# Kernel tuning notes

Hardware: AMD Instinct MI355X
Metric: run time of the kernel (lower is better)

## Reference

```python
import jax, jax.numpy as jnp
import numpy as np
from jax import lax

L_TAU = 0.8
NUM_TIME = 20
B, H, W = 128, 64, 64
FLAT = 6 * 27 * 27  # 4374 features after conv(k=10)->55x55 and maxpool2 -> 27x27

def setup_inputs() -> dict:
    key = jax.random.key(0)
    k1, k2, k3, k4, k5, k6 = jax.random.split(key, 6)
    x = jax.random.uniform(k1, (B, H * W, NUM_TIME), dtype=jnp.float32)
    y = jax.random.randint(k2, (B,), 0, 2, dtype=jnp.int64)
    Wc = jax.random.normal(k3, (6, 1, 10, 10), dtype=jnp.float32) * 0.1  # OIHW
    bc = jnp.zeros((6,), dtype=jnp.float32)
    W2 = jax.random.normal(k4, (FLAT, 2), dtype=jnp.float32) * (1.0 / np.sqrt(FLAT))
    b2 = jnp.zeros((2,), dtype=jnp.float32)
    return {"x": x, "y": y, "Wc": Wc, "bc": bc, "W2": W2, "b2": b2}

def _maxpool2(a):
    return lax.reduce_window(a, -jnp.inf, lax.max,
                             (1, 1, 2, 2), (1, 1, 2, 2), 'VALID')

def _snu_forward(x, Wc, bc, W2, b2):
    xt = jnp.transpose(x, (2, 0, 1)).reshape(NUM_TIME, B, 1, H, W)  # [T,B,1,64,64]
    s1 = jnp.zeros((B, 6, 55, 55), jnp.float32); y1 = jnp.zeros_like(s1)
    s2 = jnp.zeros((B, 2), jnp.float32);        y2 = jnp.zeros_like(s2)

    def step(carry, x_t):
        s1, y1, s2, y2 = carry
        c = lax.conv_general_dilated(x_t, Wc, (1, 1), 'VALID',
                                     dimension_numbers=('NCHW', 'OIHW', 'NCHW'))
        # SNU state: s = relu(conv(x) + l_tau * s * (1 - y)); emission: y = sigmoid(s + b)
        s1 = jax.nn.relu(c + L_TAU * s1 * (1.0 - y1))
        y1 = jax.nn.sigmoid(s1 + bc[None, :, None, None])
        h = _maxpool2(y1).reshape(B, FLAT)           # [B, 4374]
        s2 = jax.nn.relu(h @ W2 + L_TAU * s2 * (1.0 - y2))
        y2 = jax.nn.sigmoid(s2 + b2)
        return (s1, y1, s2, y2), y2

    _, outs = lax.scan(step, (s1, y1, s2, y2), xt)   # [T, B, 2]
    out_rec = jnp.concatenate([jnp.zeros((1, B, 2), jnp.float32), outs], axis=0)
    out_rec = jnp.transpose(out_rec, (1, 0, 2))      # [B, T+1, 2]
    m = jnp.sum(out_rec, axis=1) / 20.0
    return m, out_rec

def reference(x, y, Wc, bc, W2, b2):
    m, out_rec = _snu_forward(x, Wc, bc, W2, b2)
    logp = jax.nn.log_softmax(m, axis=1)
    loss = -jnp.mean(logp[jnp.arange(B), y])         # CrossEntropyLoss
    acc = jnp.mean((jnp.argmax(m, axis=1) == y).astype(jnp.float32))
    return (loss, m, out_rec, acc)
```

## Files before the change

kernel.cpp:

```cpp
#include <hip/hip_runtime.h>
#include <hip/hip_bf16.h>
#include <math.h>

#define L_TAU_C 0.8f

__device__ __forceinline__ float sigmoidf_(float x) {
    return 1.0f / (1.0f + __expf(-x));
}

__global__ __launch_bounds__(256) void k_transpose(const float* __restrict__ x,
                                                   float* __restrict__ xT) {
    int gp = blockIdx.x * 256 + threadIdx.x;
    int b = gp >> 12, p = gp & 4095;
    const float4* src = reinterpret_cast<const float4*>(x + (size_t)gp * 20);
    float v[20];
#pragma unroll
    for (int k = 0; k < 5; ++k) {
        float4 q = src[k];
        v[4 * k + 0] = q.x; v[4 * k + 1] = q.y; v[4 * k + 2] = q.z; v[4 * k + 3] = q.w;
    }
    float* dst = xT + (size_t)b * 20 * 4096 + p;
#pragma unroll
    for (int t = 0; t < 20; ++t) dst[(size_t)t * 4096] = v[t];
}

__global__ __launch_bounds__(256) void k_conv_snu(
    const float* __restrict__ xT,
    const float* __restrict__ x,
    const float* __restrict__ Wc,
    const float* __restrict__ bc,
    const float* __restrict__ W2,
    float* __restrict__ part,
    int use_xT)
{
    __shared__ float xs[64 * 68];
    __shared__ float wsh[10 * 12];
    __shared__ float red[8];

    const int tid = threadIdx.x;
    const int bi = blockIdx.x;
    const int xcd = bi & 7, slot = bi >> 3;
    const int b = (slot / 6) * 8 + xcd;
    const int ch = slot % 6;

    if (tid < 100) wsh[(tid / 10) * 12 + (tid % 10)] = Wc[ch * 100 + tid];

    const bool active = tid < 243;
    const int r = tid / 9;
    const int cg = tid % 9;
    const int row0 = r * 2, col0 = cg * 6;

    float s1[2][6], y1[2][6];
#pragma unroll
    for (int i = 0; i < 2; ++i)
#pragma unroll
        for (int j = 0; j < 6; ++j) { s1[i][j] = 0.f; y1[i][j] = 0.f; }

    const float bch = bc[ch];

    float w2r[3][2];
#pragma unroll
    for (int pj = 0; pj < 3; ++pj) { w2r[pj][0] = 0.f; w2r[pj][1] = 0.f; }
    if (active) {
        int f0 = ch * 729 + r * 27 + cg * 3;
#pragma unroll
        for (int pj = 0; pj < 3; ++pj) {
            w2r[pj][0] = W2[(size_t)(f0 + pj) * 2 + 0];
            w2r[pj][1] = W2[(size_t)(f0 + pj) * 2 + 1];
        }
    }

    for (int t = 0; t < 20; ++t) {
        __syncthreads();
        if (use_xT) {
            const float4* src = reinterpret_cast<const float4*>(
                xT + ((size_t)b * 20 + t) * 4096);
#pragma unroll
            for (int k = 0; k < 4; ++k) {
                float4 v = src[tid + k * 256];
                int p = (tid + k * 256) * 4;
                int row = p >> 6, col = p & 63;
                *reinterpret_cast<float4*>(&xs[row * 68 + col]) = v;
            }
        } else {
#pragma unroll
            for (int k = 0; k < 16; ++k) {
                int p = tid + k * 256;
                xs[(p >> 6) * 68 + (p & 63)] = x[((size_t)b * 4096 + p) * 20 + t];
            }
        }
        __syncthreads();

        float p0 = 0.f, p1 = 0.f;
        if (active) {
            float c0[6], c1[6];
#pragma unroll
            for (int j = 0; j < 6; ++j) { c0[j] = 0.f; c1[j] = 0.f; }
            float wprev[10];
#pragma unroll
            for (int xr = 0; xr < 11; ++xr) {
                float seg[15];
                const float* xrow = &xs[(row0 + xr) * 68 + col0];
#pragma unroll
                for (int j = 0; j < 15; ++j) seg[j] = xrow[j];
                float wcur[10];
                if (xr <= 9) {
#pragma unroll
                    for (int kc = 0; kc < 10; ++kc) wcur[kc] = wsh[xr * 12 + kc];
#pragma unroll
                    for (int kc = 0; kc < 10; ++kc)
#pragma unroll
                        for (int j = 0; j < 6; ++j) c0[j] += seg[j + kc] * wcur[kc];
                }
                if (xr >= 1) {
#pragma unroll
                    for (int kc = 0; kc < 10; ++kc)
#pragma unroll
                        for (int j = 0; j < 6; ++j) c1[j] += seg[j + kc] * wprev[kc];
                }
                if (xr <= 9) {
#pragma unroll
                    for (int kc = 0; kc < 10; ++kc) wprev[kc] = wcur[kc];
                }
            }
#pragma unroll
            for (int j = 0; j < 6; ++j) {
                float sa = fmaxf(c0[j] + L_TAU_C * s1[0][j] * (1.f - y1[0][j]), 0.f);
                float sb = fmaxf(c1[j] + L_TAU_C * s1[1][j] * (1.f - y1[1][j]), 0.f);
                s1[0][j] = sa; s1[1][j] = sb;
                y1[0][j] = sigmoidf_(sa + bch);
                y1[1][j] = sigmoidf_(sb + bch);
            }
#pragma unroll
            for (int pj = 0; pj < 3; ++pj) {
                float h = fmaxf(fmaxf(y1[0][2 * pj], y1[0][2 * pj + 1]),
                                fmaxf(y1[1][2 * pj], y1[1][2 * pj + 1]));
                p0 += h * w2r[pj][0];
                p1 += h * w2r[pj][1];
            }
        }
#pragma unroll
        for (int off = 32; off >= 1; off >>= 1) {
            p0 += __shfl_down(p0, off);
            p1 += __shfl_down(p1, off);
        }
        int wave = tid >> 6;
        if ((tid & 63) == 0) { red[wave * 2] = p0; red[wave * 2 + 1] = p1; }
        __syncthreads();
        if (tid == 0) {
            float q0 = red[0] + red[2] + red[4] + red[6];
            float q1 = red[1] + red[3] + red[5] + red[7];
            float* dst = part + ((size_t)t * 128 + b) * 12 + ch * 2;
            dst[0] = q0; dst[1] = q1;
        }
    }
}

__global__ __launch_bounds__(128) void k_final(const float* __restrict__ part,
                                               const void* __restrict__ yraw,
                                               const float* __restrict__ b2,
                                               float* __restrict__ out) {
    __shared__ float red[4];
    const int b = threadIdx.x;

    const int* yi = (const int*)yraw;
    bool i64 = true;
    for (int k = 0; k < 64; ++k) {
        if (yi[2 * k + 1] != 0) { i64 = false; break; }
    }
    int lbl = i64 ? (int)((const long long*)yraw)[b] : yi[b];

    float b20 = b2[0], b21 = b2[1];
    float s20 = 0.f, s21 = 0.f, y20 = 0.f, y21 = 0.f, m0 = 0.f, m1 = 0.f;
    float* orec = out + 257 + b * 42;
    orec[0] = 0.f; orec[1] = 0.f;
    for (int t = 0; t < 20; ++t) {
        const float4* pp = reinterpret_cast<const float4*>(part + ((size_t)t * 128 + b) * 12);
        float4 a = pp[0], c = pp[1], d = pp[2];
        float sum0 = a.x + a.z + c.x + c.z + d.x + d.z;
        float sum1 = a.y + a.w + c.y + c.w + d.y + d.w;
        s20 = fmaxf(sum0 + L_TAU_C * s20 * (1.f - y20), 0.f);
        s21 = fmaxf(sum1 + L_TAU_C * s21 * (1.f - y21), 0.f);
        y20 = sigmoidf_(s20 + b20);
        y21 = sigmoidf_(s21 + b21);
        orec[(t + 1) * 2 + 0] = y20;
        orec[(t + 1) * 2 + 1] = y21;
        m0 += y20; m1 += y21;
    }
    m0 *= 0.05f; m1 *= 0.05f;
    out[1 + b * 2 + 0] = m0;
    out[1 + b * 2 + 1] = m1;

    float mx = fmaxf(m0, m1);
    float lse = mx + logf(expf(m0 - mx) + expf(m1 - mx));
    float lossc = -(((lbl != 0) ? m1 : m0) - lse);
    int pred = (m1 > m0) ? 1 : 0;
    float accc = (pred == lbl) ? 1.f : 0.f;
#pragma unroll
    for (int off = 32; off >= 1; off >>= 1) {
        lossc += __shfl_down(lossc, off);
        accc += __shfl_down(accc, off);
    }
    if ((b & 63) == 0) { red[(b >> 6) * 2] = lossc; red[(b >> 6) * 2 + 1] = accc; }
    __syncthreads();
    if (b == 0) {
        out[0] = (red[0] + red[2]) * (1.f / 128.f);
        out[5633] = (red[1] + red[3]) * (1.f / 128.f);
    }
}

extern "C" void kernel_launch(void* const* d_in, const int* in_sizes, int n_in,
                              void* d_out, int out_size, void* d_ws, size_t ws_size,
                              hipStream_t stream) {
    const float* x  = (const float*)d_in[0];
    const void*  y  = d_in[1];
    const float* Wc = (const float*)d_in[2];
    const float* bc = (const float*)d_in[3];
    const float* W2 = (const float*)d_in[4];
    const float* b2 = (const float*)d_in[5];
    float* out = (float*)d_out;

    const size_t xT_floats = (size_t)128 * 20 * 4096;
    const size_t need = (xT_floats + 20 * 128 * 6 * 2) * 4;
    const int use_xT = (ws_size >= need) ? 1 : 0;

    float* xT = (float*)d_ws;
    float* part = use_xT ? ((float*)d_ws + xT_floats) : (float*)d_ws;

    if (use_xT) {
        k_transpose<<<2048, 256, 0, stream>>>(x, xT);
    }
    k_conv_snu<<<768, 256, 0, stream>>>(xT, x, Wc, bc, W2, part, use_xT);
    k_final<<<1, 128, 0, stream>>>(part, y, b2, out);
}
```

Before: 182.6 us.

## Store transposed input in fp16, widen conv tile to 8 columns with swizzled LDS

The transpose kernel now writes the time-major input copy as fp16, halving the workspace traffic, and the conv kernel converts it back to fp32 when loading shared memory. The conv tile per thread grows from 6 to 8 output columns, so a block runs 189 active threads out of 192 instead of 243 of 256. Shared memory drops its row padding in favour of an XOR swizzle with float4 reads, and the filter weights are read straight from global memory (likely scalar loads) instead of through LDS. Rounding the input to fp16 introduces precision error in the conv, and thread 188's last tile reads past the 64-column row, relying on the masked column being unused.

```diff
diff --git a/kernel.cpp b/kernel.cpp
--- a/kernel.cpp
+++ b/kernel.cpp
@@ -4,12 +4,14 @@
 
 #define L_TAU_C 0.8f
 
+typedef __attribute__((ext_vector_type(8))) _Float16 half8_t;
+
 __device__ __forceinline__ float sigmoidf_(float x) {
     return 1.0f / (1.0f + __expf(-x));
 }
 
-__global__ __launch_bounds__(256) void k_transpose(const float* __restrict__ x,
-                                                   float* __restrict__ xT) {
+__global__ __launch_bounds__(256) void k_transpose16(const float* __restrict__ x,
+                                                     _Float16* __restrict__ xT) {
     int gp = blockIdx.x * 256 + threadIdx.x;
     int b = gp >> 12, p = gp & 4095;
     const float4* src = reinterpret_cast<const float4*>(x + (size_t)gp * 20);
@@ -19,23 +21,23 @@
         float4 q = src[k];
         v[4 * k + 0] = q.x; v[4 * k + 1] = q.y; v[4 * k + 2] = q.z; v[4 * k + 3] = q.w;
     }
-    float* dst = xT + (size_t)b * 20 * 4096 + p;
-#pragma unroll
-    for (int t = 0; t < 20; ++t) dst[(size_t)t * 4096] = v[t];
-}
-
-__global__ __launch_bounds__(256) void k_conv_snu(
-    const float* __restrict__ xT,
+    _Float16* dst = xT + (size_t)b * 20 * 4096 + p;
+#pragma unroll
+    for (int t = 0; t < 20; ++t) dst[(size_t)t * 4096] = (_Float16)v[t];
+}
+
+template<int XMODE>
+__global__ __launch_bounds__(192) void k_conv_snu(
     const float* __restrict__ x,
+    const _Float16* __restrict__ xT,
     const float* __restrict__ Wc,
     const float* __restrict__ bc,
     const float* __restrict__ W2,
-    float* __restrict__ part,
-    int use_xT)
+    float* __restrict__ part)
 {
-    __shared__ float xs[64 * 68];
-    __shared__ float wsh[10 * 12];
-    __shared__ float red[8];
+    __shared__ float xs[64 * 64];
+    __shared__ float red[6];
+    float4* xs4 = reinterpret_cast<float4*>(xs);
 
     const int tid = threadIdx.x;
     const int bi = blockIdx.x;
@@ -43,88 +45,104 @@
     const int b = (slot / 6) * 8 + xcd;
     const int ch = slot % 6;
 
-    if (tid < 100) wsh[(tid / 10) * 12 + (tid % 10)] = Wc[ch * 100 + tid];
-
-    const bool active = tid < 243;
-    const int r = tid / 9;
-    const int cg = tid % 9;
-    const int row0 = r * 2, col0 = cg * 6;
-
-    float s1[2][6], y1[2][6];
+    const bool active = tid < 189;
+    const int r = tid / 7;
+    const int cg = tid % 7;
+    const int row0 = 2 * r;
+
+    float s1[2][8], y1[2][8];
 #pragma unroll
     for (int i = 0; i < 2; ++i)
 #pragma unroll
-        for (int j = 0; j < 6; ++j) { s1[i][j] = 0.f; y1[i][j] = 0.f; }
+        for (int j = 0; j < 8; ++j) { s1[i][j] = 0.f; y1[i][j] = 0.f; }
 
     const float bch = bc[ch];
 
-    float w2r[3][2];
-#pragma unroll
-    for (int pj = 0; pj < 3; ++pj) { w2r[pj][0] = 0.f; w2r[pj][1] = 0.f; }
+    float w2r[4][2];
+#pragma unroll
+    for (int pj = 0; pj < 4; ++pj) { w2r[pj][0] = 0.f; w2r[pj][1] = 0.f; }
     if (active) {
-        int f0 = ch * 729 + r * 27 + cg * 3;
-#pragma unroll
-        for (int pj = 0; pj < 3; ++pj) {
-            w2r[pj][0] = W2[(size_t)(f0 + pj) * 2 + 0];
-            w2r[pj][1] = W2[(size_t)(f0 + pj) * 2 + 1];
-        }
-    }
+#pragma unroll
+        for (int pj = 0; pj < 4; ++pj) {
+            int pc = cg * 4 + pj;
+            if (pc < 27) {
+                int f0 = ch * 729 + r * 27 + pc;
+                w2r[pj][0] = W2[(size_t)f0 * 2 + 0];
+                w2r[pj][1] = W2[(size_t)f0 * 2 + 1];
+            }
+        }
+    }
+
+    const int wave = tid >> 6, lane = tid & 63;
+    const float* wb = Wc + ch * 100;
 
     for (int t = 0; t < 20; ++t) {
         __syncthreads();
-        if (use_xT) {
-            const float4* src = reinterpret_cast<const float4*>(
-                xT + ((size_t)b * 20 + t) * 4096);
-#pragma unroll
-            for (int k = 0; k < 4; ++k) {
-                float4 v = src[tid + k * 256];
-                int p = (tid + k * 256) * 4;
-                int row = p >> 6, col = p & 63;
-                *reinterpret_cast<float4*>(&xs[row * 68 + col]) = v;
+        if (XMODE == 1) {
+            const _Float16* src = xT + ((size_t)b * 20 + t) * 4096;
+#pragma unroll
+            for (int k = 0; k < 3; ++k) {
+                int e = tid + k * 192;
+                if (e < 512) {
+                    half8_t hv = *reinterpret_cast<const half8_t*>(src + e * 8);
+                    int R = e >> 3, h = e & 7;
+                    int sw = (R >> 1) & 15;
+                    float4 fa, fb;
+                    fa.x = (float)hv[0]; fa.y = (float)hv[1];
+                    fa.z = (float)hv[2]; fa.w = (float)hv[3];
+                    fb.x = (float)hv[4]; fb.y = (float)hv[5];
+                    fb.z = (float)hv[6]; fb.w = (float)hv[7];
+                    xs4[(R << 4) + ((2 * h) ^ sw)] = fa;
+                    xs4[(R << 4) + ((2 * h + 1) ^ sw)] = fb;
+                }
             }
         } else {
-#pragma unroll
-            for (int k = 0; k < 16; ++k) {
-                int p = tid + k * 256;
-                xs[(p >> 6) * 68 + (p & 63)] = x[((size_t)b * 4096 + p) * 20 + t];
+            for (int k = 0; k < 22; ++k) {
+                int p = tid + k * 192;
+                if (p < 4096) {
+                    int R = p >> 6, c = p & 63;
+                    int sw = (R >> 1) & 15;
+                    float vv = x[((size_t)b * 4096 + p) * 20 + t];
+                    xs[(R << 6) + ((((c >> 2) ^ sw) & 15) << 2) + (c & 3)] = vv;
+                }
             }
         }
         __syncthreads();
 
         float p0 = 0.f, p1 = 0.f;
         if (active) {
-            float c0[6], c1[6];
-#pragma unroll
-            for (int j = 0; j < 6; ++j) { c0[j] = 0.f; c1[j] = 0.f; }
-            float wprev[10];
+            float c0[8], c1[8];
+#pragma unroll
+            for (int j = 0; j < 8; ++j) { c0[j] = 0.f; c1[j] = 0.f; }
+
 #pragma unroll
             for (int xr = 0; xr < 11; ++xr) {
-                float seg[15];
-                const float* xrow = &xs[(row0 + xr) * 68 + col0];
-#pragma unroll
-                for (int j = 0; j < 15; ++j) seg[j] = xrow[j];
-                float wcur[10];
+                const int R = row0 + xr;
+                const int sw = (R >> 1) & 15;
+                float4 sg[5];
+#pragma unroll
+                for (int q = 0; q < 5; ++q)
+                    sg[q] = xs4[(R << 4) + (((2 * cg + q) ^ sw) & 15)];
+                const float* seg = reinterpret_cast<const float*>(sg);
                 if (xr <= 9) {
 #pragma unroll
-                    for (int kc = 0; kc < 10; ++kc) wcur[kc] = wsh[xr * 12 + kc];
-#pragma unroll
-                    for (int kc = 0; kc < 10; ++kc)
-#pragma unroll
-                        for (int j = 0; j < 6; ++j) c0[j] += seg[j + kc] * wcur[kc];
+                    for (int kc = 0; kc < 10; ++kc) {
+                        float w = wb[xr * 10 + kc];
+#pragma unroll
+                        for (int j = 0; j < 8; ++j) c0[j] += seg[j + kc] * w;
+                    }
                 }
                 if (xr >= 1) {
 #pragma unroll
-                    for (int kc = 0; kc < 10; ++kc)
-#pragma unroll
-                        for (int j = 0; j < 6; ++j) c1[j] += seg[j + kc] * wprev[kc];
-                }
-                if (xr <= 9) {
-#pragma unroll
-                    for (int kc = 0; kc < 10; ++kc) wprev[kc] = wcur[kc];
-                }
-            }
-#pragma unroll
-            for (int j = 0; j < 6; ++j) {
+                    for (int kc = 0; kc < 10; ++kc) {
+                        float w = wb[(xr - 1) * 10 + kc];
+#pragma unroll
+                        for (int j = 0; j < 8; ++j) c1[j] += seg[j + kc] * w;
+                    }
+                }
+            }
+#pragma unroll
+            for (int j = 0; j < 8; ++j) {
                 float sa = fmaxf(c0[j] + L_TAU_C * s1[0][j] * (1.f - y1[0][j]), 0.f);
                 float sb = fmaxf(c1[j] + L_TAU_C * s1[1][j] * (1.f - y1[1][j]), 0.f);
                 s1[0][j] = sa; s1[1][j] = sb;
@@ -132,7 +150,7 @@
                 y1[1][j] = sigmoidf_(sb + bch);
             }
 #pragma unroll
-            for (int pj = 0; pj < 3; ++pj) {
+            for (int pj = 0; pj < 4; ++pj) {
                 float h = fmaxf(fmaxf(y1[0][2 * pj], y1[0][2 * pj + 1]),
                                 fmaxf(y1[1][2 * pj], y1[1][2 * pj + 1]));
                 p0 += h * w2r[pj][0];
@@ -144,12 +162,11 @@
             p0 += __shfl_down(p0, off);
             p1 += __shfl_down(p1, off);
         }
-        int wave = tid >> 6;
-        if ((tid & 63) == 0) { red[wave * 2] = p0; red[wave * 2 + 1] = p1; }
+        if (lane == 0) { red[wave * 2] = p0; red[wave * 2 + 1] = p1; }
         __syncthreads();
         if (tid == 0) {
-            float q0 = red[0] + red[2] + red[4] + red[6];
-            float q1 = red[1] + red[3] + red[5] + red[7];
+            float q0 = red[0] + red[2] + red[4];
+            float q1 = red[1] + red[3] + red[5];
             float* dst = part + ((size_t)t * 128 + b) * 12 + ch * 2;
             dst[0] = q0; dst[1] = q1;
         }
@@ -220,16 +237,18 @@
     const float* b2 = (const float*)d_in[5];
     float* out = (float*)d_out;
 
-    const size_t xT_floats = (size_t)128 * 20 * 4096;
-    const size_t need = (xT_floats + 20 * 128 * 6 * 2) * 4;
-    const int use_xT = (ws_size >= need) ? 1 : 0;
-
-    float* xT = (float*)d_ws;
-    float* part = use_xT ? ((float*)d_ws + xT_floats) : (float*)d_ws;
-
-    if (use_xT) {
-        k_transpose<<<2048, 256, 0, stream>>>(x, xT);
-    }
-    k_conv_snu<<<768, 256, 0, stream>>>(xT, x, Wc, bc, W2, part, use_xT);
+    const size_t xt_bytes = (size_t)128 * 20 * 4096 * 2;
+    const size_t part_bytes = (size_t)20 * 128 * 6 * 2 * 4;
+    const int use16 = (ws_size >= xt_bytes + part_bytes) ? 1 : 0;
+
+    _Float16* xT = (_Float16*)d_ws;
+    float* part = use16 ? (float*)((char*)d_ws + xt_bytes) : (float*)d_ws;
+
+    if (use16) {
+        k_transpose16<<<2048, 256, 0, stream>>>(x, xT);
+        k_conv_snu<1><<<768, 192, 0, stream>>>(x, xT, Wc, bc, W2, part);
+    } else {
+        k_conv_snu<0><<<768, 192, 0, stream>>>(x, (const _Float16*)d_ws, Wc, bc, W2, part);
+    }
     k_final<<<1, 128, 0, stream>>>(part, y, b2, out);
 }
```

Measured after the change: 244.5 us. 1.34x slower.
